# Performance work log

Measured on AMD Instinct MI355X. Metric: run time of the kernel, lower is better.

Reference implementation:

```python
import jax, jax.numpy as jnp
import numpy as np

DT = 0.1
N_AGENT = 262144
D_MODEL = 256
STATE_DIM = 4
UDIM = 2


def setup_inputs() -> dict:
    key = jax.random.key(0)
    ks = jax.random.split(key, 16)
    x = jax.random.normal(ks[0], (N_AGENT, D_MODEL), jnp.float32)
    tgt = jax.random.normal(ks[1], (N_AGENT, D_MODEL), jnp.float32)
    # type_index: a random partition of agents into the two dynamics types
    perm = jax.random.permutation(ks[2], N_AGENT).astype(jnp.int32)
    idx_a = perm[: N_AGENT // 2]
    idx_b = perm[N_AGENT // 2 :]
    s_in = 1.0 / np.sqrt(D_MODEL)
    s_st = 1.0 / np.sqrt(STATE_DIM)
    return {
        "x": x,
        "tgt": tgt,
        "idx_a": idx_a,
        "idx_b": idx_b,
        "W_proj_a": jax.random.normal(ks[3], (D_MODEL, UDIM), jnp.float32) * s_in,
        "b_proj_a": jnp.zeros((UDIM,), jnp.float32),
        "W_proj_b": jax.random.normal(ks[4], (D_MODEL, UDIM), jnp.float32) * s_in,
        "b_proj_b": jnp.zeros((UDIM,), jnp.float32),
        "W_f2s_a": jax.random.normal(ks[5], (D_MODEL, STATE_DIM), jnp.float32) * s_in,
        "b_f2s_a": jnp.zeros((STATE_DIM,), jnp.float32),
        "W_f2s_b": jax.random.normal(ks[6], (D_MODEL, STATE_DIM), jnp.float32) * s_in,
        "b_f2s_b": jnp.zeros((STATE_DIM,), jnp.float32),
        "W_s2f_a": jax.random.normal(ks[7], (STATE_DIM, D_MODEL), jnp.float32) * s_st,
        "b_s2f_a": jnp.zeros((D_MODEL,), jnp.float32),
        "W_s2f_b": jax.random.normal(ks[8], (STATE_DIM, D_MODEL), jnp.float32) * s_st,
        "b_s2f_b": jnp.zeros((D_MODEL,), jnp.float32),
    }


def _double_integrator_step(state, u):
    # state = [px, py, vx, vy], u = [ax, ay]; xdot = [vx, vy, ax, ay]
    deriv = jnp.concatenate([state[:, 2:4], u], axis=-1)
    return state + DT * deriv


def _unicycle_step(state, u):
    # state = [px, py, theta, v], u = [a, omega]
    th = state[:, 2]
    v = state[:, 3]
    deriv = jnp.stack([v * jnp.cos(th), v * jnp.sin(th), u[:, 1], u[:, 0]], axis=-1)
    return state + DT * deriv


def reference(x, tgt, idx_a, idx_b,
              W_proj_a, b_proj_a, W_proj_b, b_proj_b,
              W_f2s_a, b_f2s_a, W_f2s_b, b_f2s_b,
              W_s2f_a, b_s2f_a, W_s2f_b, b_s2f_b):
    out = jnp.zeros_like(tgt)
    # --- type A: double integrator --- gather -> feature2state -> proj -> step -> state2feature -> scatter
    st_a = tgt[idx_a] @ W_f2s_a + b_f2s_a            # [na, 4]
    u_a = x[idx_a] @ W_proj_a + b_proj_a             # [na, 2]
    feat_a = _double_integrator_step(st_a, u_a) @ W_s2f_a + b_s2f_a  # [na, d]
    out = out.at[idx_a].set(feat_a)
    # --- type B: unicycle ---
    st_b = tgt[idx_b] @ W_f2s_b + b_f2s_b            # [nb, 4]
    u_b = x[idx_b] @ W_proj_b + b_proj_b             # [nb, 2]
    feat_b = _unicycle_step(st_b, u_b) @ W_s2f_b + b_s2f_b           # [nb, d]
    out = out.at[idx_b].set(feat_b)
    return out
```

## Files before the change

kernel.cpp:

```cpp
#include <hip/hip_runtime.h>
#include <stdint.h>

#define DT 0.1f
#define D 256

typedef float f32x4 __attribute__((ext_vector_type(4)));

__global__ __launch_bounds__(256) void label_kernel(
    const int* __restrict__ idx_a, int n_a,
    const int* __restrict__ idx_b, int n_b,
    uint8_t* __restrict__ label)
{
    int tid = blockIdx.x * blockDim.x + threadIdx.x;
    if (tid < n_a) {
        label[idx_a[tid]] = 0;
    } else if (tid - n_a < n_b) {
        label[idx_b[tid - n_a]] = 1;
    }
}

struct WsetRegs {
    f32x4 wf0, wf1, wf2, wf3;
    f32x4 wp01, wp23;
    f32x4 ws0, ws1, ws2, ws3;
    f32x4 bs;
    float bf0, bf1, bf2, bf3;
    float bp0, bp1;
};

__device__ inline WsetRegs load_wset(int e0,
    const float* __restrict__ Wproj, const float* __restrict__ bproj,
    const float* __restrict__ Wf2s,  const float* __restrict__ bf2s,
    const float* __restrict__ Ws2f,  const float* __restrict__ bs2f)
{
    WsetRegs w;
    w.wf0  = *(const f32x4*)(Wf2s + (e0 + 0) * 4);
    w.wf1  = *(const f32x4*)(Wf2s + (e0 + 1) * 4);
    w.wf2  = *(const f32x4*)(Wf2s + (e0 + 2) * 4);
    w.wf3  = *(const f32x4*)(Wf2s + (e0 + 3) * 4);
    w.wp01 = *(const f32x4*)(Wproj + (e0 + 0) * 2);
    w.wp23 = *(const f32x4*)(Wproj + (e0 + 2) * 2);
    w.ws0  = *(const f32x4*)(Ws2f + 0 * D + e0);
    w.ws1  = *(const f32x4*)(Ws2f + 1 * D + e0);
    w.ws2  = *(const f32x4*)(Ws2f + 2 * D + e0);
    w.ws3  = *(const f32x4*)(Ws2f + 3 * D + e0);
    w.bs   = *(const f32x4*)(bs2f + e0);
    w.bf0 = bf2s[0]; w.bf1 = bf2s[1]; w.bf2 = bf2s[2]; w.bf3 = bf2s[3];
    w.bp0 = bproj[0]; w.bp1 = bproj[1];
    return w;
}

__device__ inline void reduce6(float& s0, float& s1, float& s2, float& s3,
                               float& u0, float& u1)
{
    #pragma unroll
    for (int m = 1; m < 64; m <<= 1) {
        s0 += __shfl_xor(s0, m);
        s1 += __shfl_xor(s1, m);
        s2 += __shfl_xor(s2, m);
        s3 += __shfl_xor(s3, m);
        u0 += __shfl_xor(u0, m);
        u1 += __shfl_xor(u1, m);
    }
}

template <bool UNI>
__device__ inline f32x4 compute_row(const f32x4 tg, const f32x4 xv,
                                    const WsetRegs& w)
{
    float s0 = tg.x * w.wf0.x + tg.y * w.wf1.x + tg.z * w.wf2.x + tg.w * w.wf3.x;
    float s1 = tg.x * w.wf0.y + tg.y * w.wf1.y + tg.z * w.wf2.y + tg.w * w.wf3.y;
    float s2 = tg.x * w.wf0.z + tg.y * w.wf1.z + tg.z * w.wf2.z + tg.w * w.wf3.z;
    float s3 = tg.x * w.wf0.w + tg.y * w.wf1.w + tg.z * w.wf2.w + tg.w * w.wf3.w;
    float u0 = xv.x * w.wp01.x + xv.y * w.wp01.z + xv.z * w.wp23.x + xv.w * w.wp23.z;
    float u1 = xv.x * w.wp01.y + xv.y * w.wp01.w + xv.z * w.wp23.y + xv.w * w.wp23.w;

    reduce6(s0, s1, s2, s3, u0, u1);

    s0 += w.bf0; s1 += w.bf1; s2 += w.bf2; s3 += w.bf3;
    u0 += w.bp0; u1 += w.bp1;

    if (UNI) {
        const float th = s2, v = s3;
        s0 += DT * v * __cosf(th);
        s1 += DT * v * __sinf(th);
        s2 += DT * u1;
        s3 += DT * u0;
    } else {
        s0 += DT * s2;
        s1 += DT * s3;
        s2 += DT * u0;
        s3 += DT * u1;
    }

    f32x4 o;
    o.x = w.bs.x + s0 * w.ws0.x + s1 * w.ws1.x + s2 * w.ws2.x + s3 * w.ws3.x;
    o.y = w.bs.y + s0 * w.ws0.y + s1 * w.ws1.y + s2 * w.ws2.y + s3 * w.ws3.y;
    o.z = w.bs.z + s0 * w.ws0.z + s1 * w.ws1.z + s2 * w.ws2.z + s3 * w.ws3.z;
    o.w = w.bs.w + s0 * w.ws0.w + s1 * w.ws1.w + s2 * w.ws2.w + s3 * w.ws3.w;
    return o;
}

__global__ __launch_bounds__(256) void fused_stream_kernel(
    const float* __restrict__ x,
    const float* __restrict__ tgt,
    const uint8_t* __restrict__ label,
    float* __restrict__ out,
    int n,
    const float* __restrict__ Wproj_a, const float* __restrict__ bproj_a,
    const float* __restrict__ Wf2s_a,  const float* __restrict__ bf2s_a,
    const float* __restrict__ Ws2f_a,  const float* __restrict__ bs2f_a,
    const float* __restrict__ Wproj_b, const float* __restrict__ bproj_b,
    const float* __restrict__ Wf2s_b,  const float* __restrict__ bf2s_b,
    const float* __restrict__ Ws2f_b,  const float* __restrict__ bs2f_b)
{
    const int lane  = threadIdx.x & 63;
    const int gwave = (blockIdx.x * blockDim.x + threadIdx.x) >> 6;
    const int nwave = (gridDim.x * blockDim.x) >> 6;
    const int e0 = lane << 2;

    const WsetRegs wa = load_wset(e0, Wproj_a, bproj_a, Wf2s_a, bf2s_a, Ws2f_a, bs2f_a);
    const WsetRegs wb = load_wset(e0, Wproj_b, bproj_b, Wf2s_b, bf2s_b, Ws2f_b, bs2f_b);

    for (int row = gwave; row < n; row += nwave) {
        const size_t base = (size_t)row * D + e0;
        const f32x4 tg = __builtin_nontemporal_load((const f32x4*)(tgt + base));
        const f32x4 xv = __builtin_nontemporal_load((const f32x4*)(x + base));
        const int lab = label[row];

        f32x4 o;
        if (lab == 0) {
            o = compute_row<false>(tg, xv, wa);
        } else {
            o = compute_row<true>(tg, xv, wb);
        }
        __builtin_nontemporal_store(o, (f32x4*)(out + base));
    }
}

extern "C" void kernel_launch(void* const* d_in, const int* in_sizes, int n_in,
                              void* d_out, int out_size, void* d_ws, size_t ws_size,
                              hipStream_t stream) {
    const float* x        = (const float*)d_in[0];
    const float* tgt      = (const float*)d_in[1];
    const int*   idx_a    = (const int*)d_in[2];
    const int*   idx_b    = (const int*)d_in[3];
    const float* W_proj_a = (const float*)d_in[4];
    const float* b_proj_a = (const float*)d_in[5];
    const float* W_proj_b = (const float*)d_in[6];
    const float* b_proj_b = (const float*)d_in[7];
    const float* W_f2s_a  = (const float*)d_in[8];
    const float* b_f2s_a  = (const float*)d_in[9];
    const float* W_f2s_b  = (const float*)d_in[10];
    const float* b_f2s_b  = (const float*)d_in[11];
    const float* W_s2f_a  = (const float*)d_in[12];
    const float* b_s2f_a  = (const float*)d_in[13];
    const float* W_s2f_b  = (const float*)d_in[14];
    const float* b_s2f_b  = (const float*)d_in[15];
    float* out = (float*)d_out;

    const int n_a = in_sizes[2];
    const int n_b = in_sizes[3];
    const int n   = n_a + n_b;

    uint8_t* label = (uint8_t*)d_ws;

    {
        int total = n;
        int blocks = (total + 255) / 256;
        label_kernel<<<blocks, 256, 0, stream>>>(idx_a, n_a, idx_b, n_b, label);
    }
    {
        int blocks = (n + 3) / 4;
        if (blocks > 2048) blocks = 2048;
        fused_stream_kernel<<<blocks, 256, 0, stream>>>(
            x, tgt, label, out, n,
            W_proj_a, b_proj_a, W_f2s_a, b_f2s_a, W_s2f_a, b_s2f_a,
            W_proj_b, b_proj_b, W_f2s_b, b_f2s_b, W_s2f_b, b_s2f_b);
    }
}
```

Before: 154.3 us.

## Use DPP wave reduction and software-prefetch next row in streaming kernel

Replaces the shfl_xor butterfly reduction with DPP row shifts, row broadcasts and a final readlane, which cuts the cross-lane instruction cost for the six per-row dot products. Restructures the grid-stride loop to load the next row's tgt, x and label before computing the current row, overlapping memory latency with the reduction chain. The loads also switch from nontemporal to normal loads. This costs extra registers for the prefetched data and does one redundant load on the last iteration.

```diff
diff --git a/kernel.cpp b/kernel.cpp
--- a/kernel.cpp
+++ b/kernel.cpp
@@ -17,6 +17,24 @@
     } else if (tid - n_a < n_b) {
         label[idx_b[tid - n_a]] = 1;
     }
+}
+
+template <int CTRL, int RMASK>
+__device__ __forceinline__ float dpp_mov(float x) {
+    return __builtin_bit_cast(float,
+        __builtin_amdgcn_update_dpp(0, __builtin_bit_cast(int, x),
+                                    CTRL, RMASK, 0xf, true));
+}
+
+__device__ __forceinline__ float wave_sum64(float x) {
+    x += dpp_mov<0x111, 0xf>(x);
+    x += dpp_mov<0x112, 0xf>(x);
+    x += dpp_mov<0x114, 0xf>(x);
+    x += dpp_mov<0x118, 0xf>(x);
+    x += dpp_mov<0x142, 0xa>(x);
+    x += dpp_mov<0x143, 0xc>(x);
+    return __builtin_bit_cast(float,
+        __builtin_amdgcn_readlane(__builtin_bit_cast(int, x), 63));
 }
 
 struct WsetRegs {
@@ -50,23 +68,9 @@
     return w;
 }
 
-__device__ inline void reduce6(float& s0, float& s1, float& s2, float& s3,
-                               float& u0, float& u1)
-{
-    #pragma unroll
-    for (int m = 1; m < 64; m <<= 1) {
-        s0 += __shfl_xor(s0, m);
-        s1 += __shfl_xor(s1, m);
-        s2 += __shfl_xor(s2, m);
-        s3 += __shfl_xor(s3, m);
-        u0 += __shfl_xor(u0, m);
-        u1 += __shfl_xor(u1, m);
-    }
-}
-
 template <bool UNI>
-__device__ inline f32x4 compute_row(const f32x4 tg, const f32x4 xv,
-                                    const WsetRegs& w)
+__device__ __forceinline__ f32x4 compute_row(const f32x4 tg, const f32x4 xv,
+                                             const WsetRegs& w)
 {
     float s0 = tg.x * w.wf0.x + tg.y * w.wf1.x + tg.z * w.wf2.x + tg.w * w.wf3.x;
     float s1 = tg.x * w.wf0.y + tg.y * w.wf1.y + tg.z * w.wf2.y + tg.w * w.wf3.y;
@@ -75,10 +79,12 @@
     float u0 = xv.x * w.wp01.x + xv.y * w.wp01.z + xv.z * w.wp23.x + xv.w * w.wp23.z;
     float u1 = xv.x * w.wp01.y + xv.y * w.wp01.w + xv.z * w.wp23.y + xv.w * w.wp23.w;
 
-    reduce6(s0, s1, s2, s3, u0, u1);
-
-    s0 += w.bf0; s1 += w.bf1; s2 += w.bf2; s3 += w.bf3;
-    u0 += w.bp0; u1 += w.bp1;
+    s0 = wave_sum64(s0) + w.bf0;
+    s1 = wave_sum64(s1) + w.bf1;
+    s2 = wave_sum64(s2) + w.bf2;
+    s3 = wave_sum64(s3) + w.bf3;
+    u0 = wave_sum64(u0) + w.bp0;
+    u1 = wave_sum64(u1) + w.bp1;
 
     if (UNI) {
         const float th = s2, v = s3;
@@ -122,11 +128,22 @@
     const WsetRegs wa = load_wset(e0, Wproj_a, bproj_a, Wf2s_a, bf2s_a, Ws2f_a, bs2f_a);
     const WsetRegs wb = load_wset(e0, Wproj_b, bproj_b, Wf2s_b, bf2s_b, Ws2f_b, bs2f_b);
 
-    for (int row = gwave; row < n; row += nwave) {
-        const size_t base = (size_t)row * D + e0;
-        const f32x4 tg = __builtin_nontemporal_load((const f32x4*)(tgt + base));
-        const f32x4 xv = __builtin_nontemporal_load((const f32x4*)(x + base));
-        const int lab = label[row];
+    int t = gwave;
+    if (t >= n) return;
+
+    size_t base = (size_t)t * D + e0;
+    f32x4 tg = *(const f32x4*)(tgt + base);
+    f32x4 xv = *(const f32x4*)(x + base);
+    int lab = label[t];
+
+    while (t < n) {
+        const int tn = t + nwave;
+        const int tp = (tn < n) ? tn : t;
+        const size_t baseP = (size_t)tp * D + e0;
+
+        const f32x4 tgN = *(const f32x4*)(tgt + baseP);
+        const f32x4 xvN = *(const f32x4*)(x + baseP);
+        const int labN = label[tp];
 
         f32x4 o;
         if (lab == 0) {
@@ -135,6 +152,10 @@
             o = compute_row<true>(tg, xv, wb);
         }
         __builtin_nontemporal_store(o, (f32x4*)(out + base));
+
+        t = tn;
+        base = baseP;
+        tg = tgN; xv = xvN; lab = labN;
     }
 }
 
@@ -166,8 +187,7 @@
     uint8_t* label = (uint8_t*)d_ws;
 
     {
-        int total = n;
-        int blocks = (total + 255) / 256;
+        int blocks = (n + 255) / 256;
         label_kernel<<<blocks, 256, 0, stream>>>(idx_a, n_a, idx_b, n_b, label);
     }
     {
```

After: 158.8 us. 1.03x slower.
